# Kernel tuning notes

Hardware: AMD Instinct MI355X
Metric: run time of the kernel (lower is better)

## Reference

```python
import jax, jax.numpy as jnp
import numpy as np

N_TOKEN = 4096
INPUT_DIM = 1024
QUERY_DIM = 1024
VALUE_DIM = 1024


def setup_inputs() -> dict:
    key = jax.random.key(0)
    ks = jax.random.split(key, 7)
    s = 0.02
    return {
        "x": jax.random.normal(ks[0], (N_TOKEN, INPUT_DIM), dtype=jnp.float32),
        "W_q": jax.random.normal(ks[1], (INPUT_DIM, QUERY_DIM), dtype=jnp.float32) * s,
        "b_q": jax.random.normal(ks[2], (QUERY_DIM,), dtype=jnp.float32) * s,
        "W_k": jax.random.normal(ks[3], (INPUT_DIM, QUERY_DIM), dtype=jnp.float32) * s,
        "b_k": jax.random.normal(ks[4], (QUERY_DIM,), dtype=jnp.float32) * s,
        "W_v": jax.random.normal(ks[5], (INPUT_DIM, VALUE_DIM), dtype=jnp.float32) * s,
        "b_v": jax.random.normal(ks[6], (VALUE_DIM,), dtype=jnp.float32) * s,
    }


def reference(x, W_q, b_q, W_k, b_k, W_v, b_v):
    # Projections: [n, d_in] @ [d_in, d_q/v]
    Q = x @ W_q + b_q
    K = x @ W_k + b_k
    V = x @ W_v + b_v
    n, q_dim = Q.shape
    scale = 1.0 / jnp.sqrt(jnp.asarray(q_dim, dtype=Q.dtype))
    scores = (Q @ K.T) * scale  # [n, n]
    # causal mask: positions j > i get -inf
    causal = jnp.tril(jnp.ones((n, n), dtype=bool))
    scores = jnp.where(causal, scores, -jnp.inf)
    attn = jax.nn.softmax(scores, axis=-1)
    return attn @ V
```

## Files before the change

### kernel.cpp

```cpp
#include <hip/hip_runtime.h>

#define N_TOK 4096
#define DIM   1024

typedef __bf16 bf16x8 __attribute__((ext_vector_type(8)));
typedef float  f32x4  __attribute__((ext_vector_type(4)));

__device__ __forceinline__ unsigned short f2bf(float f) {
  union { float f; unsigned u; } v; v.f = f;
  unsigned u = v.u;
  return (unsigned short)((u + 0x7fffu + ((u >> 16) & 1u)) >> 16);
}
__device__ __forceinline__ float bf2f(unsigned short h) {
  union { unsigned u; float f; } v; v.u = ((unsigned)h) << 16;
  return v.f;
}

__device__ __forceinline__ void gll16(const unsigned short* g,
                                      unsigned short* l) {
  __builtin_amdgcn_global_load_lds(
      (const __attribute__((address_space(1))) unsigned int*)g,
      (__attribute__((address_space(3))) unsigned int*)l, 16, 0, 0);
}

#define PB_CVT 0
#define PB_TQ 2048
#define PB_ZERO 5120
#define PB_LSUM 6016
#define PB_BIAS 6020
#define PB_TOTAL 6023

__global__ void prep(const float* __restrict__ x, const float* __restrict__ Wq,
                     const float* __restrict__ Wk, const float* __restrict__ Wv,
                     const float* __restrict__ bq, const float* __restrict__ bk,
                     const float* __restrict__ bv,
                     unsigned short* __restrict__ xb,
                     unsigned short* __restrict__ Wt,
                     float* __restrict__ out, float* __restrict__ ball,
                     float* __restrict__ Lsum) {
  const int b = blockIdx.x;
  const int t = threadIdx.x;
  if (b < PB_TQ) {
    const int i = ((b - PB_CVT) * 256 + t) * 8;
    float4 v0 = *(const float4*)(x + i);
    float4 v1 = *(const float4*)(x + i + 4);
    ushort4 r0, r1;
    r0.x = f2bf(v0.x); r0.y = f2bf(v0.y); r0.z = f2bf(v0.z); r0.w = f2bf(v0.w);
    r1.x = f2bf(v1.x); r1.y = f2bf(v1.y); r1.z = f2bf(v1.z); r1.w = f2bf(v1.w);
    *(ushort4*)(xb + i) = r0;
    *(ushort4*)(xb + i + 4) = r1;
  } else if (b < PB_ZERO) {
    const int which = (b - PB_TQ) >> 10;
    const int lb = (b - PB_TQ) & 1023;
    const float* W = (which == 0) ? Wq : (which == 1) ? Wk : Wv;
    unsigned short* D = Wt + (size_t)which * 1024 * 1024;
    __shared__ float tile[32][33];
    const int bx = (lb & 31) * 32, by = (lb >> 5) * 32;
    const int tx = t & 31, ty = t >> 5;
    for (int r = ty; r < 32; r += 8)
      tile[r][tx] = W[(size_t)(by + r) * DIM + bx + tx];
    __syncthreads();
    for (int r = ty; r < 32; r += 8)
      D[(size_t)(bx + r) * DIM + by + tx] = f2bf(tile[tx][r]);
  } else if (b < PB_LSUM) {
    float4* p = (float4*)(out + (size_t)512 * DIM);
    const int i = ((b - PB_ZERO) * 256 + t) * 4;
#pragma unroll
    for (int c = 0; c < 4; c++) p[i + c] = make_float4(0.f, 0.f, 0.f, 0.f);
  } else if (b < PB_BIAS) {
    const int i = ((b - PB_LSUM) * 256 + t) * 4;
    *(float4*)(Lsum + i) = make_float4(0.f, 0.f, 0.f, 0.f);
  } else {
    const int i = ((b - PB_BIAS) * 256 + t) * 4;
#pragma unroll
    for (int c = 0; c < 4; c++) {
      const int k = i + c;
      if (k < 3072)
        ball[k] = (k < 1024) ? bq[k] * 0.03125f
                             : ((k < 2048) ? bk[k - 1024] : bv[k - 2048]);
    }
  }
}

#define BK 64

template <int EPI>
__global__ void gemm_tn(const unsigned short* __restrict__ A,
                        const unsigned short* __restrict__ B,
                        void* __restrict__ Cout,
                        const float* __restrict__ bias,
                        float* __restrict__ Lsum,
                        unsigned short* __restrict__ VT,
                        int K, int lda, int ldb, int ldc) {
  int bm, bn, kbeg, kend;
  bool single = true;
  if (EPI == 3) {
    const int i = blockIdx.x;
    bn = i & 7;
    const int q = i >> 3;
    int b = (int)((sqrtf(2.f * (float)q + 1.f) - 1.f) * 0.5f);
    while (2 * (b + 1) * (b + 2) <= q) ++b;
    while (2 * b * (b + 1) > q) --b;
    const int r = q - 2 * b * (b + 1);
    bm = 4 * b + (r & 3);
    const int z = r >> 2;
    const int Keff = (bm + 1) * 128;
    kbeg = z * 512;
    kend = min(kbeg + 512, Keff);
    single = (Keff <= 512);
  } else if (EPI == 2) {
    const int id = blockIdx.x;
    const int wg = (id & 7) * 66 + (id >> 3);
    float s = sqrtf(8.f * (float)wg + 1.f);
    bm = (int)((s - 1.f) * 0.5f);
    while ((bm + 1) * (bm + 2) / 2 <= wg) ++bm;
    while (bm * (bm + 1) / 2 > wg) --bm;
    bn = wg - bm * (bm + 1) / 2;
    kbeg = 0; kend = K;
  } else {
    const int id = blockIdx.y * gridDim.x + blockIdx.x;
    const int wg = (id & 7) * 96 + (id >> 3);
    bm = wg / 24; bn = wg % 24;
    kbeg = 0; kend = K;
  }

  __shared__ __align__(16) unsigned short smA[128 * 64];
  __shared__ __align__(16) unsigned short smB[128 * 64];

  const int t = threadIdx.x;
  const int lane = t & 63, w = t >> 6;
  const int wm = (w & 1) * 64, wn = (w >> 1) * 64;

  f32x4 acc[4][4] = {};

  const unsigned short* Ab = A + (size_t)bm * 128 * lda;
  const unsigned short* Bb = B + (size_t)bn * 128 * ldb;

  const int rA = wm + (lane & 15);
  const int rB = wn + (lane & 15);
  const int kquad = (lane >> 4) << 3;
  const int swz = (lane & 7) << 3;

  const int lr = lane >> 3;
  const int g8 = ((lane & 7) ^ lr) << 3;
  const unsigned short* pa = Ab + (size_t)lr * lda + g8 + kbeg;
  const unsigned short* pb = Bb + (size_t)lr * ldb + g8 + kbeg;

  for (int k0 = kbeg; k0 < kend; k0 += BK) {
    __syncthreads();
#pragma unroll
    for (int m = 0; m < 4; m++) {
      const int r0 = (w << 5) + (m << 3);
      gll16(pa + (size_t)r0 * lda, smA + r0 * 64);
      gll16(pb + (size_t)r0 * ldb, smB + r0 * 64);
    }
    pa += BK; pb += BK;
    __syncthreads();

#pragma unroll
    for (int kk = 0; kk < BK; kk += 32) {
      bf16x8 af[4], bfr[4];
      const int kof = (kk + kquad) ^ swz;
#pragma unroll
      for (int i = 0; i < 4; i++)
        af[i] = *(const bf16x8*)(&smA[(rA + i * 16) * 64 + kof]);
#pragma unroll
      for (int j = 0; j < 4; j++)
        bfr[j] = *(const bf16x8*)(&smB[(rB + j * 16) * 64 + kof]);
#pragma unroll
      for (int i = 0; i < 4; i++)
#pragma unroll
        for (int j = 0; j < 4; j++)
          acc[i][j] = __builtin_amdgcn_mfma_f32_16x16x32_bf16(af[i], bfr[j],
                                                              acc[i][j], 0, 0, 0);
    }
  }

  float* Cf = (float*)Cout;
  unsigned short* Ch = (unsigned short*)Cout;
  const int colbase = bn * 128 + wn + (lane & 15);
  const int rowbase = bm * 128 + wm + ((lane >> 4) << 2);

  if (EPI == 0) {
    const bool isV = (bn >= 16);
#pragma unroll
    for (int i = 0; i < 4; i++)
#pragma unroll
      for (int j = 0; j < 4; j++) {
        const int gc = colbase + j * 16;
        const float cs = (gc < 1024) ? 0.03125f : 1.0f;
        const float bs = bias[gc];
        ushort4 h4;
        unsigned short* hp = (unsigned short*)&h4;
#pragma unroll
        for (int r = 0; r < 4; r++) {
          const int gr = rowbase + i * 16 + r;
          const unsigned short h = f2bf(acc[i][j][r] * cs + bs);
          Ch[(size_t)gr * ldc + gc] = h;
          hp[r] = h;
        }
        if (isV) {
          const int gr0 = rowbase + i * 16;
          *(ushort4*)(VT + (size_t)(gc - 2048) * N_TOK + gr0) = h4;
        }
      }
  } else if (EPI == 2) {
    __syncthreads();
    float* Lp = (float*)smA;
    if (t < 128) Lp[t] = 0.f;
    __syncthreads();
#pragma unroll
    for (int i = 0; i < 4; i++)
#pragma unroll
      for (int r = 0; r < 4; r++) {
        const int gr = rowbase + i * 16 + r;
        float sj = 0.f;
#pragma unroll
        for (int j = 0; j < 4; j++) {
          const int gc = colbase + j * 16;
          unsigned short h = 0;
          if (gc <= gr) h = f2bf(__expf(acc[i][j][r]));
          Ch[(size_t)gr * ldc + gc] = h;
          sj += bf2f(h);
        }
        sj += __shfl_xor(sj, 1);
        sj += __shfl_xor(sj, 2);
        sj += __shfl_xor(sj, 4);
        sj += __shfl_xor(sj, 8);
        if ((lane & 15) == 0)
          atomicAdd(&Lp[wm + ((lane >> 4) << 2) + i * 16 + r], sj);
      }
    __syncthreads();
    if (t < 128) atomicAdd(&Lsum[bm * 128 + t], Lp[t]);
  } else {
#pragma unroll
    for (int i = 0; i < 4; i++)
#pragma unroll
      for (int r = 0; r < 4; r++) {
        const int gr = rowbase + i * 16 + r;
        const float linv = 1.0f / Lsum[gr];
#pragma unroll
        for (int j = 0; j < 4; j++) {
          const int gc = colbase + j * 16;
          const float v = acc[i][j][r] * linv;
          if (single)
            Cf[(size_t)gr * ldc + gc] = v;
          else
            atomicAdd(&Cf[(size_t)gr * ldc + gc], v);
        }
      }
  }
}

extern "C" void kernel_launch(void* const* d_in, const int* in_sizes, int n_in,
                              void* d_out, int out_size, void* d_ws,
                              size_t ws_size, hipStream_t stream) {
  (void)in_sizes; (void)n_in; (void)out_size; (void)ws_size;
  const float* x  = (const float*)d_in[0];
  const float* Wq = (const float*)d_in[1];
  const float* bq = (const float*)d_in[2];
  const float* Wk = (const float*)d_in[3];
  const float* bk = (const float*)d_in[4];
  const float* Wv = (const float*)d_in[5];
  const float* bv = (const float*)d_in[6];
  float* out = (float*)d_out;

  const size_t M1 = (size_t)1024 * 1024;
  unsigned short* xb   = (unsigned short*)d_ws;
  unsigned short* Wt   = xb + 4 * M1;
  unsigned short* Call = Wt + 3 * M1;
  unsigned short* Sb   = Call + 12 * M1;
  float* ball          = (float*)(Sb + 16 * M1);
  float* Lsum          = ball + 3072;

  prep<<<PB_TOTAL, 256, 0, stream>>>(x, Wq, Wk, Wv, bq, bk, bv, xb, Wt, out,
                                     ball, Lsum);
  gemm_tn<0><<<dim3(24, 32), 256, 0, stream>>>(xb, Wt, Call, ball, nullptr,
                                               xb, DIM, DIM, DIM, 3 * DIM);
  gemm_tn<2><<<528, 256, 0, stream>>>(Call, Call + 1024, Sb, nullptr, Lsum,
                                      nullptr, DIM, 3 * DIM, 3 * DIM, N_TOK);
  gemm_tn<3><<<1152, 256, 0, stream>>>(Sb, xb, out, nullptr, Lsum, nullptr,
                                       N_TOK, N_TOK, N_TOK, DIM);
}
```

Measured before the change: 222.7 us.

## Replace atomic split-K accumulation in PV GEMM with partial buffers and reduce kernel

The attention-times-V GEMM now splits K in 1024-wide chunks instead of 512, so fewer blocks are launched (640 instead of 1152). Extra K splits write to a partial buffer (aliased onto the weight workspace) rather than atomically adding into the output, and a new reduce kernel sums them into the output. This removes the output zeroing pass in prep and the float atomics, but adds a kernel launch and extra partial-buffer traffic. Larger K chunks also reduce parallelism for the long rows. The x bf16 staging buffer is moved into the score buffer region.

```diff
diff --git a/kernel.cpp b/kernel.cpp
--- a/kernel.cpp
+++ b/kernel.cpp
@@ -25,19 +25,17 @@
 
 #define PB_CVT 0
 #define PB_TQ 2048
-#define PB_ZERO 5120
-#define PB_LSUM 6016
-#define PB_BIAS 6020
-#define PB_TOTAL 6023
+#define PB_LSUM 5120
+#define PB_BIAS 5124
+#define PB_TOTAL 5127
 
 __global__ void prep(const float* __restrict__ x, const float* __restrict__ Wq,
                      const float* __restrict__ Wk, const float* __restrict__ Wv,
                      const float* __restrict__ bq, const float* __restrict__ bk,
                      const float* __restrict__ bv,
-                     unsigned short* __restrict__ xb,
+                     unsigned short* __restrict__ xs,
                      unsigned short* __restrict__ Wt,
-                     float* __restrict__ out, float* __restrict__ ball,
-                     float* __restrict__ Lsum) {
+                     float* __restrict__ ball, float* __restrict__ Lsum) {
   const int b = blockIdx.x;
   const int t = threadIdx.x;
   if (b < PB_TQ) {
@@ -47,9 +45,9 @@
     ushort4 r0, r1;
     r0.x = f2bf(v0.x); r0.y = f2bf(v0.y); r0.z = f2bf(v0.z); r0.w = f2bf(v0.w);
     r1.x = f2bf(v1.x); r1.y = f2bf(v1.y); r1.z = f2bf(v1.z); r1.w = f2bf(v1.w);
-    *(ushort4*)(xb + i) = r0;
-    *(ushort4*)(xb + i + 4) = r1;
-  } else if (b < PB_ZERO) {
+    *(ushort4*)(xs + i) = r0;
+    *(ushort4*)(xs + i + 4) = r1;
+  } else if (b < PB_LSUM) {
     const int which = (b - PB_TQ) >> 10;
     const int lb = (b - PB_TQ) & 1023;
     const float* W = (which == 0) ? Wq : (which == 1) ? Wk : Wv;
@@ -62,11 +60,6 @@
     __syncthreads();
     for (int r = ty; r < 32; r += 8)
       D[(size_t)(bx + r) * DIM + by + tx] = f2bf(tile[tx][r]);
-  } else if (b < PB_LSUM) {
-    float4* p = (float4*)(out + (size_t)512 * DIM);
-    const int i = ((b - PB_ZERO) * 256 + t) * 4;
-#pragma unroll
-    for (int c = 0; c < 4; c++) p[i + c] = make_float4(0.f, 0.f, 0.f, 0.f);
   } else if (b < PB_BIAS) {
     const int i = ((b - PB_LSUM) * 256 + t) * 4;
     *(float4*)(Lsum + i) = make_float4(0.f, 0.f, 0.f, 0.f);
@@ -91,23 +84,24 @@
                         const float* __restrict__ bias,
                         float* __restrict__ Lsum,
                         unsigned short* __restrict__ VT,
+                        float* __restrict__ Part,
                         int K, int lda, int ldb, int ldc) {
   int bm, bn, kbeg, kend;
-  bool single = true;
+  int zz = 0, pidx = 0;
   if (EPI == 3) {
     const int i = blockIdx.x;
     bn = i & 7;
     const int q = i >> 3;
-    int b = (int)((sqrtf(2.f * (float)q + 1.f) - 1.f) * 0.5f);
-    while (2 * (b + 1) * (b + 2) <= q) ++b;
-    while (2 * b * (b + 1) > q) --b;
-    const int r = q - 2 * b * (b + 1);
-    bm = 4 * b + (r & 3);
-    const int z = r >> 2;
+    if (q < 8)       { bm = q;                    zz = 0; }
+    else if (q < 24) { bm = 8 + ((q - 8) >> 1);   zz = (q - 8) & 1; }
+    else if (q < 48) { bm = 16 + (q - 24) / 3;    zz = (q - 24) % 3; }
+    else             { bm = 24 + ((q - 48) >> 2); zz = (q - 48) & 3; }
     const int Keff = (bm + 1) * 128;
-    kbeg = z * 512;
-    kend = min(kbeg + 512, Keff);
-    single = (Keff <= 512);
+    kbeg = zz * 1024;
+    kend = min(kbeg + 1024, Keff);
+    pidx = (bm < 16) ? (bm - 8)
+         : (bm < 24) ? 8 + (bm - 16) * 2 + (zz - 1)
+                     : 24 + (bm - 24) * 3 + (zz - 1);
   } else if (EPI == 2) {
     const int id = blockIdx.x;
     const int wg = (id & 7) * 66 + (id >> 3);
@@ -233,22 +227,44 @@
     __syncthreads();
     if (t < 128) atomicAdd(&Lsum[bm * 128 + t], Lp[t]);
   } else {
+    float* dst = (zz == 0) ? (Cf + (size_t)bm * 128 * 1024)
+                           : (Part + (size_t)pidx * 131072);
+    const int colloc = bn * 128 + wn + (lane & 15);
+    const int rowloc = wm + ((lane >> 4) << 2);
 #pragma unroll
     for (int i = 0; i < 4; i++)
 #pragma unroll
       for (int r = 0; r < 4; r++) {
-        const int gr = rowbase + i * 16 + r;
-        const float linv = 1.0f / Lsum[gr];
-#pragma unroll
-        for (int j = 0; j < 4; j++) {
-          const int gc = colbase + j * 16;
-          const float v = acc[i][j][r] * linv;
-          if (single)
-            Cf[(size_t)gr * ldc + gc] = v;
-          else
-            atomicAdd(&Cf[(size_t)gr * ldc + gc], v);
-        }
+        const int rr = rowloc + i * 16 + r;
+        const float linv = 1.0f / Lsum[bm * 128 + rr];
+#pragma unroll
+        for (int j = 0; j < 4; j++)
+          dst[(size_t)rr * 1024 + colloc + j * 16] = acc[i][j][r] * linv;
       }
+  }
+}
+
+__global__ void reduce_out(const float* __restrict__ Part,
+                           float* __restrict__ out) {
+  const int bm = 8 + blockIdx.x;
+  const int sub = blockIdx.y;
+  const int extra = (bm < 16) ? 1 : (bm < 24) ? 2 : 3;
+  const int pbase = (bm < 16) ? (bm - 8)
+                  : (bm < 24) ? 8 + (bm - 16) * 2
+                              : 24 + (bm - 24) * 3;
+  const int t = threadIdx.x;
+  float4* po = (float4*)(out + (size_t)(bm * 128 + sub * 4) * 1024);
+  const float4* pp = (const float4*)(Part + (size_t)pbase * 131072 +
+                                     (size_t)sub * 4096);
+#pragma unroll
+  for (int k = 0; k < 4; k++) {
+    const int idx = t + k * 256;
+    float4 v = po[idx];
+    for (int e = 0; e < extra; e++) {
+      const float4 q = pp[(size_t)e * 32768 + idx];
+      v.x += q.x; v.y += q.y; v.z += q.z; v.w += q.w;
+    }
+    po[idx] = v;
   }
 }
 
@@ -272,13 +288,18 @@
   unsigned short* Sb   = Call + 12 * M1;
   float* ball          = (float*)(Sb + 16 * M1);
   float* Lsum          = ball + 3072;
-
-  prep<<<PB_TOTAL, 256, 0, stream>>>(x, Wq, Wk, Wv, bq, bk, bv, xb, Wt, out,
+  unsigned short* xs   = Sb;
+  float* Part          = (float*)Wt;
+
+  prep<<<PB_TOTAL, 256, 0, stream>>>(x, Wq, Wk, Wv, bq, bk, bv, xs, Wt,
                                      ball, Lsum);
-  gemm_tn<0><<<dim3(24, 32), 256, 0, stream>>>(xb, Wt, Call, ball, nullptr,
-                                               xb, DIM, DIM, DIM, 3 * DIM);
+  gemm_tn<0><<<dim3(24, 32), 256, 0, stream>>>(xs, Wt, Call, ball, nullptr,
+                                               xb, nullptr, DIM, DIM, DIM,
+                                               3 * DIM);
   gemm_tn<2><<<528, 256, 0, stream>>>(Call, Call + 1024, Sb, nullptr, Lsum,
-                                      nullptr, DIM, 3 * DIM, 3 * DIM, N_TOK);
-  gemm_tn<3><<<1152, 256, 0, stream>>>(Sb, xb, out, nullptr, Lsum, nullptr,
-                                       N_TOK, N_TOK, N_TOK, DIM);
-}
+                                      nullptr, nullptr, DIM, 3 * DIM, 3 * DIM,
+                                      N_TOK);
+  gemm_tn<3><<<640, 256, 0, stream>>>(Sb, xb, out, nullptr, Lsum, nullptr,
+                                      Part, N_TOK, N_TOK, N_TOK, DIM);
+  reduce_out<<<dim3(24, 32), 256, 0, stream>>>(Part, out);
+}
```

Result: faster. 184.8 us (median of 2 runs) (-17.0%).
